# Kernel optimization log

Hardware: AMD Instinct MI355X
Metric: run time of the kernel (lower is better)

## Reference

```python
import jax, jax.numpy as jnp
from jax import lax
import numpy as np

EPS = 1e-5

def chan_ln(x, g, b):
    # LayerNorm over channel dim of NCHW
    mu = jnp.mean(x, axis=1, keepdims=True)
    var = jnp.mean((x - mu) ** 2, axis=1, keepdims=True)
    return (x - mu) / jnp.sqrt(var + EPS) * g[None, :, None, None] + b[None, :, None, None]

def selective_scan(dts, Bs, Cs, us, A):
    # dts, us: (B,K,C,L); Bs, Cs: (B,K,N,L); A: (K,C,N)
    def step(h, inp):
        dt_t, B_t, C_t, u_t = inp
        dA = jnp.exp(dt_t[..., None] * A)                     # (B,K,C,N)
        h = h * dA + (dt_t * u_t)[..., None] * B_t[:, :, None, :]
        y = jnp.einsum('bkcn,bkn->bkc', h, C_t)
        return h, y
    h0 = jnp.zeros(dts.shape[:-1] + (A.shape[-1],), dts.dtype)
    seq = (jnp.moveaxis(dts, -1, 0), jnp.moveaxis(Bs, -1, 0),
           jnp.moveaxis(Cs, -1, 0), jnp.moveaxis(us, -1, 0))
    _, ys = lax.scan(step, h0, seq)
    return jnp.moveaxis(ys, 0, -1)                            # (B,K,C,L)

def ss2d_core(x, x_proj_w, dt_proj_w, dt_proj_b, A_log, Ds):
    Bb, C, H, W = x.shape
    L = H * W
    R = dt_proj_w.shape[-1]
    N = A_log.shape[-1]
    x_flat = x.reshape(Bb, C, L)
    x_tr = jnp.transpose(x, (0, 1, 3, 2)).reshape(Bb, C, L)
    x_hwwh = jnp.stack([x_flat, x_tr], axis=1)                # (B,2,C,L)
    xs = jnp.concatenate([x_hwwh, jnp.flip(x_hwwh, axis=-1)], axis=1)  # (B,4,C,L)
    x_dbl = jnp.einsum('bkcl,kdc->bkdl', xs, x_proj_w)        # d = R+2N
    dts, Bs, Cs = jnp.split(x_dbl, [R, R + N], axis=2)
    dts = jnp.einsum('bkrl,kcr->bkcl', dts, dt_proj_w) + dt_proj_b[None, :, :, None]
    dts = jax.nn.softplus(dts)
    A = -jnp.exp(A_log)
    ys = selective_scan(dts, Bs, Cs, xs, A)
    ys = ys + xs * Ds[None, :, :, None]
    y0 = ys[:, 0]
    y1 = jnp.transpose(ys[:, 1].reshape(Bb, C, W, H), (0, 1, 3, 2)).reshape(Bb, C, L)
    yi = jnp.flip(ys[:, 2:], axis=-1)
    y2 = yi[:, 0]
    y3 = jnp.transpose(yi[:, 1].reshape(Bb, C, W, H), (0, 1, 3, 2)).reshape(Bb, C, L)
    return (y0 + y1 + y2 + y3).reshape(Bb, C, H, W)

def setup_inputs() -> dict:
    key = jax.random.key(0)
    ks = jax.random.split(key, 12)
    Hd, Di, N, R = 96, 192, 16, 6
    B, HH, WW = 2, 64, 64
    s = 0.02
    inp = {}
    inp['x'] = jax.random.normal(ks[0], (B, Hd, HH, WW), jnp.float32)
    inp['in_conv_w'] = s * jax.random.normal(ks[1], (Hd, Hd), jnp.float32)
    inp['ln1_g'] = jnp.ones((Hd,), jnp.float32)
    inp['ln1_b'] = jnp.zeros((Hd,), jnp.float32)
    inp['in_proj_w'] = s * jax.random.normal(ks[2], (Di, Hd), jnp.float32)
    inp['dw_w'] = s * jax.random.normal(ks[3], (Di, 1, 3, 3), jnp.float32)
    inp['dw_b'] = jnp.zeros((Di,), jnp.float32)
    inp['x_proj_w'] = s * jax.random.normal(ks[4], (4, R + 2 * N, Di), jnp.float32)
    inp['dt_proj_w'] = s * jax.random.normal(ks[5], (4, Di, R), jnp.float32)
    inp['dt_proj_b'] = 0.01 * jax.random.normal(ks[6], (4, Di), jnp.float32)
    inp['A_log'] = jnp.log(jnp.broadcast_to(jnp.arange(1.0, N + 1.0, dtype=jnp.float32), (4, Di, N)))
    inp['Ds'] = jnp.ones((4, Di), jnp.float32)
    inp['out_norm_g'] = jnp.ones((Di,), jnp.float32)
    inp['out_norm_b'] = jnp.zeros((Di,), jnp.float32)
    inp['out_proj_w'] = s * jax.random.normal(ks[7], (Hd, Di), jnp.float32)
    inp['skip_scale'] = jnp.ones((1,), jnp.float32)
    return inp

def reference(x, in_conv_w, ln1_g, ln1_b, in_proj_w, dw_w, dw_b, x_proj_w,
              dt_proj_w, dt_proj_b, A_log, Ds, out_norm_g, out_norm_b,
              out_proj_w, skip_scale):
    x1 = jnp.einsum('oi,bihw->bohw', in_conv_w, x)            # in_conv 1x1
    x1 = chan_ln(x1, ln1_g, ln1_b)
    skip = x1
    h = jnp.einsum('oi,bihw->bohw', in_proj_w, x1)            # in_proj 1x1
    h = lax.conv_general_dilated(h, dw_w, (1, 1), 'SAME',
                                 dimension_numbers=('NCHW', 'OIHW', 'NCHW'),
                                 feature_group_count=h.shape[1])
    h = h + dw_b[None, :, None, None]
    h = jax.nn.silu(h)
    y = ss2d_core(h, x_proj_w, dt_proj_w, dt_proj_b, A_log, Ds)
    y = chan_ln(y, out_norm_g, out_norm_b)
    out = jnp.einsum('oi,bihw->bohw', out_proj_w, y)
    return out + skip * skip_scale[0]
```

## Files before the change

kernel.cpp:

```cpp
#include <hip/hip_runtime.h>
#include <hip/hip_bf16.h>

#define Bb 2
#define HD 96
#define DI 192
#define LL 4096
#define Kd 4
#define Ns 16
#define Rr 6
#define SEG 256
#define SEGLEN 16
#define NBKCN (Bb*Kd*DI*Ns)
#define LNEPS 1e-5f
#define RW 40
#define LOG2E 1.44269504f

__global__ __launch_bounds__(384) void k_fused_in(const float* __restrict__ x,
    const float* __restrict__ w1, const float* __restrict__ g, const float* __restrict__ be,
    const float* __restrict__ w2, float* __restrict__ x1, float* __restrict__ hp) {
  __shared__ float xs[16][100];
  __shared__ float t1[16][100];
  __shared__ float red[2][16][24];
  int t = threadIdx.x;
  int l0 = blockIdx.x*16; int b = blockIdx.y;
  for (int idx=t; idx<HD*16; idx+=384) {
    int c = idx>>4, i = idx&15;
    xs[i][c] = x[((size_t)b*HD + c)*LL + l0 + i];
  }
  __syncthreads();
  int l = t & 15, cg = t >> 4;
  float a0=0.f,a1=0.f,a2=0.f,a3=0.f;
  {
    const float4* xr = (const float4*)&xs[l][0];
    const float4* wr0 = (const float4*)(w1 + (size_t)(cg*4+0)*HD);
    const float4* wr1 = (const float4*)(w1 + (size_t)(cg*4+1)*HD);
    const float4* wr2 = (const float4*)(w1 + (size_t)(cg*4+2)*HD);
    const float4* wr3 = (const float4*)(w1 + (size_t)(cg*4+3)*HD);
    #pragma unroll 6
    for (int j=0;j<24;j++) {
      float4 xv = xr[j];
      float4 v0 = wr0[j], v1 = wr1[j], v2 = wr2[j], v3 = wr3[j];
      a0 += xv.x*v0.x + xv.y*v0.y + xv.z*v0.z + xv.w*v0.w;
      a1 += xv.x*v1.x + xv.y*v1.y + xv.z*v1.z + xv.w*v1.w;
      a2 += xv.x*v2.x + xv.y*v2.y + xv.z*v2.z + xv.w*v2.w;
      a3 += xv.x*v3.x + xv.y*v3.y + xv.z*v3.z + xv.w*v3.w;
    }
  }
  float s = a0+a1+a2+a3;
  float s2 = a0*a0+a1*a1+a2*a2+a3*a3;
  red[0][l][cg]=s; red[1][l][cg]=s2;
  __syncthreads();
  float S=0.f, S2=0.f;
  #pragma unroll
  for (int q=0;q<24;q++) { S += red[0][l][q]; S2 += red[1][l][q]; }
  float mu = S*(1.f/HD);
  float var = S2*(1.f/HD) - mu*mu;
  float r = rsqrtf(var + LNEPS);
  {
    int c0 = cg*4;
    float v0 = (a0-mu)*r*g[c0+0] + be[c0+0];
    float v1 = (a1-mu)*r*g[c0+1] + be[c0+1];
    float v2 = (a2-mu)*r*g[c0+2] + be[c0+2];
    float v3 = (a3-mu)*r*g[c0+3] + be[c0+3];
    t1[l][c0+0]=v0; t1[l][c0+1]=v1; t1[l][c0+2]=v2; t1[l][c0+3]=v3;
    size_t ob = ((size_t)b*HD + c0)*LL + l0 + l;
    x1[ob]=v0; x1[ob+LL]=v1; x1[ob+2*(size_t)LL]=v2; x1[ob+3*(size_t)LL]=v3;
  }
  __syncthreads();
  float acc[8];
  #pragma unroll
  for (int q=0;q<8;q++) acc[q]=0.f;
  {
    const float4* yr = (const float4*)&t1[l][0];
    #pragma unroll 4
    for (int j=0;j<24;j++) {
      float4 yv = yr[j];
      #pragma unroll
      for (int q=0;q<8;q++) {
        float4 wv = ((const float4*)(w2 + (size_t)(cg*8+q)*HD))[j];
        acc[q] += yv.x*wv.x + yv.y*wv.y + yv.z*wv.z + yv.w*wv.w;
      }
    }
  }
  #pragma unroll
  for (int q=0;q<8;q++)
    hp[((size_t)b*DI + cg*8+q)*LL + l0 + l] = acc[q];
}

__global__ __launch_bounds__(192) void k_dwconv_silu_t(const float* __restrict__ hp,
    const float* __restrict__ wgt, const float* __restrict__ bias, float* __restrict__ v_t) {
  __shared__ float lds[24*65];
  int t = threadIdx.x;
  int w0 = t & 63, dg = t >> 6;
  int h = blockIdx.x, dq = blockIdx.y, b = blockIdx.z;
  for (int dd=0; dd<8; ++dd) {
    int dl = dg*8 + dd;
    int d = dq*24 + dl;
    const float* src = hp + ((size_t)b*DI + d)*LL;
    const float* wk = wgt + d*9;
    float acc = bias[d];
    #pragma unroll
    for (int dy=-1; dy<=1; dy++) {
      int hh = h+dy;
      if (hh < 0 || hh >= 64) continue;
      #pragma unroll
      for (int dx=-1; dx<=1; dx++) {
        int ww = w0+dx;
        if (ww < 0 || ww >= 64) continue;
        acc += wk[(dy+1)*3 + (dx+1)] * src[hh*64 + ww];
      }
    }
    lds[dl*65 + w0] = acc / (1.f + __expf(-acc));
  }
  __syncthreads();
  int hc = t % 24, ig = t / 24;
  if (ig < 8) {
    for (int ii=0; ii<8; ii++) {
      int i = ig*8 + ii;
      v_t[((size_t)b*LL + h*64 + i)*DI + dq*24 + hc] = lds[hc*65 + i];
    }
  }
}

__global__ __launch_bounds__(512) void k_proj(const float* __restrict__ v_t,
    const float* __restrict__ xpw, float* __restrict__ dblp) {
  __shared__ float lds[64*196];
  int t = threadIdx.x;
  int pt = blockIdx.x, k = blockIdx.y, b = blockIdx.z;
  const float4* src = (const float4*)(v_t + ((size_t)b*LL + pt*64)*DI);
  for (int idx=t; idx<64*48; idx+=512) {
    int p = idx/48, q = idx - p*48;
    *((float4*)&lds[p*196 + 4*q]) = src[idx];
  }
  __syncthreads();
  int p = t & 63, dg = t >> 6;
  int d0 = (dg<6) ? dg*5 : 30 + (dg-6)*4;
  int nd = (dg<6) ? 5 : 4;
  float acc[5];
  #pragma unroll
  for (int q=0;q<5;q++) acc[q]=0.f;
  const float4* W4 = (const float4*)(xpw + (size_t)(k*38 + d0)*DI);
  const float4* row4 = (const float4*)(lds + p*196);
  for (int c4=0;c4<48;c4++) {
    float4 xv = row4[c4];
    #pragma unroll
    for (int dd=0;dd<5;dd++) {
      if (dd < nd) {
        float4 wv = W4[(size_t)dd*48 + c4];
        acc[dd] += xv.x*wv.x + xv.y*wv.y + xv.z*wv.z + xv.w*wv.w;
      }
    }
  }
  float* o = dblp + (((size_t)b*4 + k)*LL + pt*64 + p)*RW;
  for (int dd=0;dd<nd;dd++) {
    int d = d0 + dd;
    o[d + ((d>=6)?2:0)] = acc[dd];
  }
}

__device__ __forceinline__ void dir_map(int k, int s, int& pbase, int& pstr) {
  if (k==0)      { pbase = s*16;                          pstr = 1;   }
  else if (k==1) { pbase = (s&3)*1024 + (s>>2);           pstr = 64;  }
  else if (k==2) { pbase = 4095 - s*16;                   pstr = -1;  }
  else           { pbase = 4095 - (s&3)*1024 - (s>>2);    pstr = -64; }
}

__device__ __forceinline__ float softplus_f(float raw) {
  float e = __expf(raw);
  float l = __logf(1.f + e);
  return (raw > 20.f) ? raw : l;
}

__global__ __launch_bounds__(384) void k_scanA(const float* __restrict__ v_t,
    const float* __restrict__ dblp, const float* __restrict__ dtw,
    const float* __restrict__ dtb, const float* __restrict__ A_log,
    float* __restrict__ hend, float* __restrict__ sdt_o) {
  __shared__ float uld[2][SEGLEN][DI];
  __shared__ float rows[2][SEGLEN][24];
  int t = threadIdx.x;
  int sub = t/192, tl = t - sub*192;
  int s = blockIdx.x*2 + sub;
  int k = blockIdx.y, b = blockIdx.z;
  int bk = b*4 + k;
  int pbase, pstr; dir_map(k, s, pbase, pstr);
  #pragma unroll
  for (int i=0;i<4;i++) {
    int idx = tl + i*192;
    int row = idx/48, q = idx - row*48;
    int p = pbase + row*pstr;
    const float4* src = (const float4*)(v_t + ((size_t)b*LL + p)*DI) + q;
    *((float4*)&uld[sub][row][4*q]) = *src;
  }
  if (tl < 96) {
    int r = tl/6, q = tl - r*6;
    const float4* src = (const float4*)(dblp + ((size_t)bk*LL + pbase + r*pstr)*RW);
    *((float4*)&rows[sub][r][4*q]) = src[q];
  }
  int c = tl;
  float w[6];
  {
    const float* wr = dtw + ((size_t)k*DI + c)*Rr;
    #pragma unroll
    for (int r=0;r<6;r++) w[r] = wr[r];
  }
  float bias = dtb[k*DI + c];
  float A2[16];
  {
    const float4* Ap = (const float4*)(A_log + ((size_t)k*DI + c)*Ns);
    #pragma unroll
    for (int q=0;q<4;q++) {
      float4 av = Ap[q];
      A2[4*q+0]=-__expf(av.x)*LOG2E; A2[4*q+1]=-__expf(av.y)*LOG2E;
      A2[4*q+2]=-__expf(av.z)*LOG2E; A2[4*q+3]=-__expf(av.w)*LOG2E;
    }
  }
  __syncthreads();
  float dtv[SEGLEN], duv[SEGLEN];
  float sdt = 0.f;
  #pragma unroll
  for (int j=0;j<SEGLEN;j++) {
    const float* row = &rows[sub][j][0];
    float4 d0 = *((const float4*)row);
    float2 d1 = *((const float2*)(row+4));
    float raw = bias + w[0]*d0.x + w[1]*d0.y + w[2]*d0.z + w[3]*d0.w
              + w[4]*d1.x + w[5]*d1.y;
    float dt = softplus_f(raw);
    dtv[j] = dt;
    duv[j] = dt * uld[sub][j][c];
    sdt += dt;
  }
  float h[16];
  #pragma unroll
  for (int n=0;n<16;n++) h[n]=0.f;
  #pragma unroll
  for (int j=0;j<SEGLEN;j++) {
    float dt = dtv[j], du = duv[j];
    const float4* Bv = (const float4*)(&rows[sub][j][8]);
    #pragma unroll
    for (int q=0;q<4;q++) {
      float4 bv = Bv[q];
      h[4*q+0] = h[4*q+0]*__builtin_amdgcn_exp2f(dt*A2[4*q+0]) + du*bv.x;
      h[4*q+1] = h[4*q+1]*__builtin_amdgcn_exp2f(dt*A2[4*q+1]) + du*bv.y;
      h[4*q+2] = h[4*q+2]*__builtin_amdgcn_exp2f(dt*A2[4*q+2]) + du*bv.z;
      h[4*q+3] = h[4*q+3]*__builtin_amdgcn_exp2f(dt*A2[4*q+3]) + du*bv.w;
    }
  }
  float* ho = hend + ((size_t)s*8 + bk)*(DI*Ns) + c;
  #pragma unroll
  for (int n=0;n<16;n++) ho[(size_t)n*DI] = h[n];
  sdt_o[((size_t)s*8 + bk)*DI + c] = sdt;
}

__global__ __launch_bounds__(64) void k_fix(float* __restrict__ hend,
    const float* __restrict__ sdt, const float* __restrict__ A_log) {
  int t = blockIdx.x*64 + threadIdx.x;
  int c = t % DI;
  int nn = (t / DI) & 15;
  int bk = t / (DI*Ns);
  int k = bk & 3;
  float A = -__expf(A_log[((size_t)k*DI + c)*Ns + nn]);
  float hi = 0.f;
  #pragma unroll 8
  for (int s=0; s<SEG; s++) {
    float he = hend[(size_t)s*NBKCN + t];
    float P  = __expf(A * sdt[(size_t)s*(8*DI) + bk*DI + c]);
    hend[(size_t)s*NBKCN + t] = hi;
    hi = he + P*hi;
  }
}

__global__ __launch_bounds__(384) void k_scanB(const float* __restrict__ v_t,
    const float* __restrict__ dblp, const float* __restrict__ dtw,
    const float* __restrict__ dtb, const float* __restrict__ A_log,
    const float* __restrict__ hinit, float* __restrict__ ym) {
  __shared__ float uld[2][SEGLEN][DI];
  __shared__ float rows[2][SEGLEN][RW];
  int t = threadIdx.x;
  int sub = t/192, tl = t - sub*192;
  int s = blockIdx.x*2 + sub;
  int k = blockIdx.y, b = blockIdx.z;
  int bk = b*4 + k;
  int pbase, pstr; dir_map(k, s, pbase, pstr);
  #pragma unroll
  for (int i=0;i<4;i++) {
    int idx = tl + i*192;
    int row = idx/48, q = idx - row*48;
    int p = pbase + row*pstr;
    const float4* src = (const float4*)(v_t + ((size_t)b*LL + p)*DI) + q;
    *((float4*)&uld[sub][row][4*q]) = *src;
  }
  if (tl < 160) {
    int r = tl/10, q = tl - r*10;
    const float4* src = (const float4*)(dblp + ((size_t)bk*LL + pbase + r*pstr)*RW);
    *((float4*)&rows[sub][r][4*q]) = src[q];
  }
  int c = tl;
  float w[6];
  {
    const float* wr = dtw + ((size_t)k*DI + c)*Rr;
    #pragma unroll
    for (int r=0;r<6;r++) w[r] = wr[r];
  }
  float bias = dtb[k*DI + c];
  float A2[16];
  {
    const float4* Ap = (const float4*)(A_log + ((size_t)k*DI + c)*Ns);
    #pragma unroll
    for (int q=0;q<4;q++) {
      float4 av = Ap[q];
      A2[4*q+0]=-__expf(av.x)*LOG2E; A2[4*q+1]=-__expf(av.y)*LOG2E;
      A2[4*q+2]=-__expf(av.z)*LOG2E; A2[4*q+3]=-__expf(av.w)*LOG2E;
    }
  }
  float h[16];
  {
    const float* hi = hinit + ((size_t)s*8 + bk)*(DI*Ns) + c;
    #pragma unroll
    for (int n=0;n<16;n++) h[n] = hi[(size_t)n*DI];
  }
  __syncthreads();
  float dtv[SEGLEN], duv[SEGLEN];
  #pragma unroll
  for (int j=0;j<SEGLEN;j++) {
    const float* row = &rows[sub][j][0];
    float4 d0 = *((const float4*)row);
    float2 d1 = *((const float2*)(row+4));
    float raw = bias + w[0]*d0.x + w[1]*d0.y + w[2]*d0.z + w[3]*d0.w
              + w[4]*d1.x + w[5]*d1.y;
    float dt = softplus_f(raw);
    dtv[j] = dt;
    duv[j] = dt * uld[sub][j][c];
  }
  float* ymk = ym + ((size_t)(k*Bb + b)*LL)*DI;
  #pragma unroll
  for (int j=0;j<SEGLEN;j++) {
    float dt = dtv[j], du = duv[j];
    const float4* Bv = (const float4*)(&rows[sub][j][8]);
    const float4* Cv = (const float4*)(&rows[sub][j][24]);
    float y = 0.f;
    #pragma unroll
    for (int q=0;q<4;q++) {
      float4 bv = Bv[q];
      float4 cv = Cv[q];
      h[4*q+0] = h[4*q+0]*__builtin_amdgcn_exp2f(dt*A2[4*q+0]) + du*bv.x;
      h[4*q+1] = h[4*q+1]*__builtin_amdgcn_exp2f(dt*A2[4*q+1]) + du*bv.y;
      h[4*q+2] = h[4*q+2]*__builtin_amdgcn_exp2f(dt*A2[4*q+2]) + du*bv.z;
      h[4*q+3] = h[4*q+3]*__builtin_amdgcn_exp2f(dt*A2[4*q+3]) + du*bv.w;
      y += h[4*q+0]*cv.x + h[4*q+1]*cv.y + h[4*q+2]*cv.z + h[4*q+3]*cv.w;
    }
    int p = pbase + j*pstr;
    ymk[(size_t)p*DI + c] = y;
  }
}

__global__ __launch_bounds__(384) void k_merge_out(const float* __restrict__ ym,
    const float* __restrict__ v_t, const float* __restrict__ Ds,
    const float* __restrict__ g, const float* __restrict__ be,
    const float* __restrict__ w3, const float* __restrict__ x1,
    const float* __restrict__ ss, float* __restrict__ out) {
  __shared__ float tile2[16*196];
  __shared__ float red[2][16][6];
  int t = threadIdx.x;
  int b = blockIdx.y;
  int l0 = blockIdx.x*16;
  int pp = t / 192, c = t - pp*192;
  int wv = t >> 6;
  int ln = t & 63;
  float sd = Ds[c] + Ds[DI+c] + Ds[2*DI+c] + Ds[3*DI+c];
  float gg = g[c], bb = be[c];
  float v[8];
  #pragma unroll
  for (int j=0;j<8;j++) {
    int i = 2*j + pp;
    size_t row = ((size_t)b*LL + l0 + i)*DI + c;
    float vv = ym[row] + ym[(size_t)2*LL*DI + row]
             + ym[(size_t)4*LL*DI + row] + ym[(size_t)6*LL*DI + row]
             + v_t[row]*sd;
    v[j] = vv;
    float s = vv, s2 = vv*vv;
    #pragma unroll
    for (int d=1; d<64; d<<=1) { s += __shfl_xor(s,d); s2 += __shfl_xor(s2,d); }
    if (ln==0) { red[0][i][wv]=s; red[1][i][wv]=s2; }
  }
  __syncthreads();
  #pragma unroll
  for (int j=0;j<8;j++) {
    int i = 2*j + pp;
    int w0i = pp*3;
    float S  = red[0][i][w0i]+red[0][i][w0i+1]+red[0][i][w0i+2];
    float S2 = red[1][i][w0i]+red[1][i][w0i+1]+red[1][i][w0i+2];
    float mu = S*(1.f/DI);
    float var = S2*(1.f/DI) - mu*mu;
    float r = rsqrtf(var + LNEPS);
    tile2[i*196 + c] = (v[j]-mu)*r*gg + bb;
  }
  __syncthreads();
  int l = t & 15, og = t >> 4;
  float a0=0.f,a1=0.f,a2=0.f,a3=0.f;
  {
    const float4* yr = (const float4*)&tile2[l*196];
    const float4* wr0 = (const float4*)(w3 + (size_t)(og*4+0)*DI);
    const float4* wr1 = (const float4*)(w3 + (size_t)(og*4+1)*DI);
    const float4* wr2 = (const float4*)(w3 + (size_t)(og*4+2)*DI);
    const float4* wr3 = (const float4*)(w3 + (size_t)(og*4+3)*DI);
    #pragma unroll 6
    for (int j=0;j<48;j++) {
      float4 yv = yr[j];
      float4 v0 = wr0[j], v1 = wr1[j], v2 = wr2[j], v3 = wr3[j];
      a0 += yv.x*v0.x + yv.y*v0.y + yv.z*v0.z + yv.w*v0.w;
      a1 += yv.x*v1.x + yv.y*v1.y + yv.z*v1.z + yv.w*v1.w;
      a2 += yv.x*v2.x + yv.y*v2.y + yv.z*v2.z + yv.w*v2.w;
      a3 += yv.x*v3.x + yv.y*v3.y + yv.z*v3.z + yv.w*v3.w;
    }
  }
  float sc = ss[0];
  int o0 = og*4;
  size_t ob = ((size_t)b*HD + o0)*LL + l0 + l;
  out[ob]            = a0 + x1[ob]*sc;
  out[ob+LL]         = a1 + x1[ob+LL]*sc;
  out[ob+2*(size_t)LL] = a2 + x1[ob+2*(size_t)LL]*sc;
  out[ob+3*(size_t)LL] = a3 + x1[ob+3*(size_t)LL]*sc;
}

extern "C" void kernel_launch(void* const* d_in, const int* in_sizes, int n_in,
                              void* d_out, int out_size, void* d_ws, size_t ws_size,
                              hipStream_t stream) {
  const float* x         = (const float*)d_in[0];
  const float* in_conv_w = (const float*)d_in[1];
  const float* ln1_g     = (const float*)d_in[2];
  const float* ln1_b     = (const float*)d_in[3];
  const float* in_proj_w = (const float*)d_in[4];
  const float* dw_w      = (const float*)d_in[5];
  const float* dw_b      = (const float*)d_in[6];
  const float* x_proj_w  = (const float*)d_in[7];
  const float* dt_proj_w = (const float*)d_in[8];
  const float* dt_proj_b = (const float*)d_in[9];
  const float* A_log     = (const float*)d_in[10];
  const float* Ds        = (const float*)d_in[11];
  const float* onorm_g   = (const float*)d_in[12];
  const float* onorm_b   = (const float*)d_in[13];
  const float* out_proj_w= (const float*)d_in[14];
  const float* skip_s    = (const float*)d_in[15];
  float* out = (float*)d_out;

  float* ws   = (float*)d_ws;
  float* x1   = ws;
  float* hp   = x1   + 786432;
  float* v_t  = hp   + 1572864;
  float* dblp = v_t  + 1572864;
  float* hend = dblp + 1310720;
  float* sdt  = hend + 6291456;
  float* ym   = sdt  + 393216;

  k_fused_in<<<dim3(LL/16, Bb), dim3(384), 0, stream>>>(x, in_conv_w, ln1_g, ln1_b, in_proj_w, x1, hp);
  k_dwconv_silu_t<<<dim3(64, 8, Bb), dim3(192), 0, stream>>>(hp, dw_w, dw_b, v_t);
  k_proj   <<<dim3(LL/64, Kd, Bb), dim3(512), 0, stream>>>(v_t, x_proj_w, dblp);
  k_scanA  <<<dim3(SEG/2, Kd, Bb), dim3(384), 0, stream>>>(v_t, dblp, dt_proj_w, dt_proj_b, A_log, hend, sdt);
  k_fix    <<<dim3(NBKCN/64), dim3(64), 0, stream>>>(hend, sdt, A_log);
  k_scanB  <<<dim3(SEG/2, Kd, Bb), dim3(384), 0, stream>>>(v_t, dblp, dt_proj_w, dt_proj_b, A_log, hend, ym);
  k_merge_out<<<dim3(LL/16, Bb), dim3(384), 0, stream>>>(ym, v_t, Ds, onorm_g, onorm_b, out_proj_w, x1, skip_s, out);
}
```

Measured before the change: 278.0 us.

## Merge scan phases into one cooperative persistent kernel with grid syncs

The three scan kernels (segment-local scan, cross-segment carry fix, and the final scan with output) are fused into one cooperative kernel. It launches 512 blocks of 192 threads that loop over tasks and are separated by grid.sync(). This removes two kernel launch boundaries. In exchange it adds grid-wide barrier cost and a fixed grid size that may underuse the GPU, especially in the fix phase, which has only NBKCN/192 threads' worth of work spread across the grid.

```diff
diff --git a/kernel.cpp b/kernel.cpp
--- a/kernel.cpp
+++ b/kernel.cpp
@@ -1,5 +1,8 @@
 #include <hip/hip_runtime.h>
+#include <hip/hip_cooperative_groups.h>
 #include <hip/hip_bf16.h>
+
+namespace cg = cooperative_groups;
 
 #define Bb 2
 #define HD 96
@@ -10,6 +13,7 @@
 #define Rr 6
 #define SEG 256
 #define SEGLEN 16
+#define NTASK (SEG*Kd*Bb)
 #define NBKCN (Bb*Kd*DI*Ns)
 #define LNEPS 1e-5f
 #define RW 40
@@ -28,14 +32,14 @@
     xs[i][c] = x[((size_t)b*HD + c)*LL + l0 + i];
   }
   __syncthreads();
-  int l = t & 15, cg = t >> 4;
+  int l = t & 15, cg0 = t >> 4;
   float a0=0.f,a1=0.f,a2=0.f,a3=0.f;
   {
     const float4* xr = (const float4*)&xs[l][0];
-    const float4* wr0 = (const float4*)(w1 + (size_t)(cg*4+0)*HD);
-    const float4* wr1 = (const float4*)(w1 + (size_t)(cg*4+1)*HD);
-    const float4* wr2 = (const float4*)(w1 + (size_t)(cg*4+2)*HD);
-    const float4* wr3 = (const float4*)(w1 + (size_t)(cg*4+3)*HD);
+    const float4* wr0 = (const float4*)(w1 + (size_t)(cg0*4+0)*HD);
+    const float4* wr1 = (const float4*)(w1 + (size_t)(cg0*4+1)*HD);
+    const float4* wr2 = (const float4*)(w1 + (size_t)(cg0*4+2)*HD);
+    const float4* wr3 = (const float4*)(w1 + (size_t)(cg0*4+3)*HD);
     #pragma unroll 6
     for (int j=0;j<24;j++) {
       float4 xv = xr[j];
@@ -48,7 +52,7 @@
   }
   float s = a0+a1+a2+a3;
   float s2 = a0*a0+a1*a1+a2*a2+a3*a3;
-  red[0][l][cg]=s; red[1][l][cg]=s2;
+  red[0][l][cg0]=s; red[1][l][cg0]=s2;
   __syncthreads();
   float S=0.f, S2=0.f;
   #pragma unroll
@@ -57,7 +61,7 @@
   float var = S2*(1.f/HD) - mu*mu;
   float r = rsqrtf(var + LNEPS);
   {
-    int c0 = cg*4;
+    int c0 = cg0*4;
     float v0 = (a0-mu)*r*g[c0+0] + be[c0+0];
     float v1 = (a1-mu)*r*g[c0+1] + be[c0+1];
     float v2 = (a2-mu)*r*g[c0+2] + be[c0+2];
@@ -77,14 +81,14 @@
       float4 yv = yr[j];
       #pragma unroll
       for (int q=0;q<8;q++) {
-        float4 wv = ((const float4*)(w2 + (size_t)(cg*8+q)*HD))[j];
+        float4 wv = ((const float4*)(w2 + (size_t)(cg0*8+q)*HD))[j];
         acc[q] += yv.x*wv.x + yv.y*wv.y + yv.z*wv.z + yv.w*wv.w;
       }
     }
   }
   #pragma unroll
   for (int q=0;q<8;q++)
-    hp[((size_t)b*DI + cg*8+q)*LL + l0 + l] = acc[q];
+    hp[((size_t)b*DI + cg0*8+q)*LL + l0 + l] = acc[q];
 }
 
 __global__ __launch_bounds__(192) void k_dwconv_silu_t(const float* __restrict__ hp,
@@ -171,185 +175,179 @@
   return (raw > 20.f) ? raw : l;
 }
 
-__global__ __launch_bounds__(384) void k_scanA(const float* __restrict__ v_t,
-    const float* __restrict__ dblp, const float* __restrict__ dtw,
-    const float* __restrict__ dtb, const float* __restrict__ A_log,
-    float* __restrict__ hend, float* __restrict__ sdt_o) {
-  __shared__ float uld[2][SEGLEN][DI];
-  __shared__ float rows[2][SEGLEN][24];
+__global__ __launch_bounds__(192, 3) void k_scan_all(
+    const float* __restrict__ v_t, const float* __restrict__ dblp,
+    const float* __restrict__ dtw, const float* __restrict__ dtb,
+    const float* __restrict__ A_log, float* __restrict__ hend,
+    float* __restrict__ sdt_o, float* __restrict__ ym) {
+  cg::grid_group grid = cg::this_grid();
+  __shared__ float uld[SEGLEN][DI];
+  __shared__ float rows[SEGLEN][RW];
   int t = threadIdx.x;
-  int sub = t/192, tl = t - sub*192;
-  int s = blockIdx.x*2 + sub;
-  int k = blockIdx.y, b = blockIdx.z;
-  int bk = b*4 + k;
-  int pbase, pstr; dir_map(k, s, pbase, pstr);
-  #pragma unroll
-  for (int i=0;i<4;i++) {
-    int idx = tl + i*192;
-    int row = idx/48, q = idx - row*48;
-    int p = pbase + row*pstr;
-    const float4* src = (const float4*)(v_t + ((size_t)b*LL + p)*DI) + q;
-    *((float4*)&uld[sub][row][4*q]) = *src;
-  }
-  if (tl < 96) {
-    int r = tl/6, q = tl - r*6;
-    const float4* src = (const float4*)(dblp + ((size_t)bk*LL + pbase + r*pstr)*RW);
-    *((float4*)&rows[sub][r][4*q]) = src[q];
-  }
-  int c = tl;
-  float w[6];
-  {
-    const float* wr = dtw + ((size_t)k*DI + c)*Rr;
-    #pragma unroll
-    for (int r=0;r<6;r++) w[r] = wr[r];
-  }
-  float bias = dtb[k*DI + c];
-  float A2[16];
-  {
-    const float4* Ap = (const float4*)(A_log + ((size_t)k*DI + c)*Ns);
-    #pragma unroll
-    for (int q=0;q<4;q++) {
-      float4 av = Ap[q];
-      A2[4*q+0]=-__expf(av.x)*LOG2E; A2[4*q+1]=-__expf(av.y)*LOG2E;
-      A2[4*q+2]=-__expf(av.z)*LOG2E; A2[4*q+3]=-__expf(av.w)*LOG2E;
-    }
-  }
-  __syncthreads();
-  float dtv[SEGLEN], duv[SEGLEN];
-  float sdt = 0.f;
-  #pragma unroll
-  for (int j=0;j<SEGLEN;j++) {
-    const float* row = &rows[sub][j][0];
-    float4 d0 = *((const float4*)row);
-    float2 d1 = *((const float2*)(row+4));
-    float raw = bias + w[0]*d0.x + w[1]*d0.y + w[2]*d0.z + w[3]*d0.w
-              + w[4]*d1.x + w[5]*d1.y;
-    float dt = softplus_f(raw);
-    dtv[j] = dt;
-    duv[j] = dt * uld[sub][j][c];
-    sdt += dt;
-  }
-  float h[16];
-  #pragma unroll
-  for (int n=0;n<16;n++) h[n]=0.f;
-  #pragma unroll
-  for (int j=0;j<SEGLEN;j++) {
-    float dt = dtv[j], du = duv[j];
-    const float4* Bv = (const float4*)(&rows[sub][j][8]);
-    #pragma unroll
-    for (int q=0;q<4;q++) {
-      float4 bv = Bv[q];
-      h[4*q+0] = h[4*q+0]*__builtin_amdgcn_exp2f(dt*A2[4*q+0]) + du*bv.x;
-      h[4*q+1] = h[4*q+1]*__builtin_amdgcn_exp2f(dt*A2[4*q+1]) + du*bv.y;
-      h[4*q+2] = h[4*q+2]*__builtin_amdgcn_exp2f(dt*A2[4*q+2]) + du*bv.z;
-      h[4*q+3] = h[4*q+3]*__builtin_amdgcn_exp2f(dt*A2[4*q+3]) + du*bv.w;
-    }
-  }
-  float* ho = hend + ((size_t)s*8 + bk)*(DI*Ns) + c;
-  #pragma unroll
-  for (int n=0;n<16;n++) ho[(size_t)n*DI] = h[n];
-  sdt_o[((size_t)s*8 + bk)*DI + c] = sdt;
-}
-
-__global__ __launch_bounds__(64) void k_fix(float* __restrict__ hend,
-    const float* __restrict__ sdt, const float* __restrict__ A_log) {
-  int t = blockIdx.x*64 + threadIdx.x;
-  int c = t % DI;
-  int nn = (t / DI) & 15;
-  int bk = t / (DI*Ns);
-  int k = bk & 3;
-  float A = -__expf(A_log[((size_t)k*DI + c)*Ns + nn]);
-  float hi = 0.f;
-  #pragma unroll 8
-  for (int s=0; s<SEG; s++) {
-    float he = hend[(size_t)s*NBKCN + t];
-    float P  = __expf(A * sdt[(size_t)s*(8*DI) + bk*DI + c]);
-    hend[(size_t)s*NBKCN + t] = hi;
-    hi = he + P*hi;
-  }
-}
-
-__global__ __launch_bounds__(384) void k_scanB(const float* __restrict__ v_t,
-    const float* __restrict__ dblp, const float* __restrict__ dtw,
-    const float* __restrict__ dtb, const float* __restrict__ A_log,
-    const float* __restrict__ hinit, float* __restrict__ ym) {
-  __shared__ float uld[2][SEGLEN][DI];
-  __shared__ float rows[2][SEGLEN][RW];
-  int t = threadIdx.x;
-  int sub = t/192, tl = t - sub*192;
-  int s = blockIdx.x*2 + sub;
-  int k = blockIdx.y, b = blockIdx.z;
-  int bk = b*4 + k;
-  int pbase, pstr; dir_map(k, s, pbase, pstr);
-  #pragma unroll
-  for (int i=0;i<4;i++) {
-    int idx = tl + i*192;
-    int row = idx/48, q = idx - row*48;
-    int p = pbase + row*pstr;
-    const float4* src = (const float4*)(v_t + ((size_t)b*LL + p)*DI) + q;
-    *((float4*)&uld[sub][row][4*q]) = *src;
-  }
-  if (tl < 160) {
-    int r = tl/10, q = tl - r*10;
-    const float4* src = (const float4*)(dblp + ((size_t)bk*LL + pbase + r*pstr)*RW);
-    *((float4*)&rows[sub][r][4*q]) = src[q];
-  }
-  int c = tl;
-  float w[6];
-  {
-    const float* wr = dtw + ((size_t)k*DI + c)*Rr;
-    #pragma unroll
-    for (int r=0;r<6;r++) w[r] = wr[r];
-  }
-  float bias = dtb[k*DI + c];
-  float A2[16];
-  {
-    const float4* Ap = (const float4*)(A_log + ((size_t)k*DI + c)*Ns);
-    #pragma unroll
-    for (int q=0;q<4;q++) {
-      float4 av = Ap[q];
-      A2[4*q+0]=-__expf(av.x)*LOG2E; A2[4*q+1]=-__expf(av.y)*LOG2E;
-      A2[4*q+2]=-__expf(av.z)*LOG2E; A2[4*q+3]=-__expf(av.w)*LOG2E;
-    }
-  }
-  float h[16];
-  {
-    const float* hi = hinit + ((size_t)s*8 + bk)*(DI*Ns) + c;
-    #pragma unroll
-    for (int n=0;n<16;n++) h[n] = hi[(size_t)n*DI];
-  }
-  __syncthreads();
-  float dtv[SEGLEN], duv[SEGLEN];
-  #pragma unroll
-  for (int j=0;j<SEGLEN;j++) {
-    const float* row = &rows[sub][j][0];
-    float4 d0 = *((const float4*)row);
-    float2 d1 = *((const float2*)(row+4));
-    float raw = bias + w[0]*d0.x + w[1]*d0.y + w[2]*d0.z + w[3]*d0.w
-              + w[4]*d1.x + w[5]*d1.y;
-    float dt = softplus_f(raw);
-    dtv[j] = dt;
-    duv[j] = dt * uld[sub][j][c];
-  }
-  float* ymk = ym + ((size_t)(k*Bb + b)*LL)*DI;
-  #pragma unroll
-  for (int j=0;j<SEGLEN;j++) {
-    float dt = dtv[j], du = duv[j];
-    const float4* Bv = (const float4*)(&rows[sub][j][8]);
-    const float4* Cv = (const float4*)(&rows[sub][j][24]);
-    float y = 0.f;
-    #pragma unroll
-    for (int q=0;q<4;q++) {
-      float4 bv = Bv[q];
-      float4 cv = Cv[q];
-      h[4*q+0] = h[4*q+0]*__builtin_amdgcn_exp2f(dt*A2[4*q+0]) + du*bv.x;
-      h[4*q+1] = h[4*q+1]*__builtin_amdgcn_exp2f(dt*A2[4*q+1]) + du*bv.y;
-      h[4*q+2] = h[4*q+2]*__builtin_amdgcn_exp2f(dt*A2[4*q+2]) + du*bv.z;
-      h[4*q+3] = h[4*q+3]*__builtin_amdgcn_exp2f(dt*A2[4*q+3]) + du*bv.w;
-      y += h[4*q+0]*cv.x + h[4*q+1]*cv.y + h[4*q+2]*cv.z + h[4*q+3]*cv.w;
-    }
-    int p = pbase + j*pstr;
-    ymk[(size_t)p*DI + c] = y;
+  int c = t;
+
+  for (int task = blockIdx.x; task < NTASK; task += gridDim.x) {
+    int s = task & (SEG-1);
+    int k = (task >> 8) & 3;
+    int b = task >> 10;
+    int bk = b*4 + k;
+    int pbase, pstr; dir_map(k, s, pbase, pstr);
+    __syncthreads();
+    #pragma unroll
+    for (int i=0;i<4;i++) {
+      int idx = t + i*192;
+      int row = idx/48, q = idx - row*48;
+      int p = pbase + row*pstr;
+      *((float4*)&uld[row][4*q]) = ((const float4*)(v_t + ((size_t)b*LL + p)*DI))[q];
+    }
+    if (t < 96) {
+      int r = t/6, q = t - r*6;
+      *((float4*)&rows[r][4*q]) = ((const float4*)(dblp + ((size_t)bk*LL + pbase + r*pstr)*RW))[q];
+    }
+    float w[6];
+    {
+      const float* wr = dtw + ((size_t)k*DI + c)*Rr;
+      #pragma unroll
+      for (int r=0;r<6;r++) w[r] = wr[r];
+    }
+    float bias = dtb[k*DI + c];
+    float A2[16];
+    {
+      const float4* Ap = (const float4*)(A_log + ((size_t)k*DI + c)*Ns);
+      #pragma unroll
+      for (int q=0;q<4;q++) {
+        float4 av = Ap[q];
+        A2[4*q+0]=-__expf(av.x)*LOG2E; A2[4*q+1]=-__expf(av.y)*LOG2E;
+        A2[4*q+2]=-__expf(av.z)*LOG2E; A2[4*q+3]=-__expf(av.w)*LOG2E;
+      }
+    }
+    __syncthreads();
+    float dtv[SEGLEN], duv[SEGLEN];
+    float sdt = 0.f;
+    #pragma unroll
+    for (int j=0;j<SEGLEN;j++) {
+      const float* row = &rows[j][0];
+      float4 d0 = *((const float4*)row);
+      float2 d1 = *((const float2*)(row+4));
+      float raw = bias + w[0]*d0.x + w[1]*d0.y + w[2]*d0.z + w[3]*d0.w
+                + w[4]*d1.x + w[5]*d1.y;
+      float dt = softplus_f(raw);
+      dtv[j] = dt;
+      duv[j] = dt * uld[j][c];
+      sdt += dt;
+    }
+    float h[16];
+    #pragma unroll
+    for (int n=0;n<16;n++) h[n]=0.f;
+    #pragma unroll
+    for (int j=0;j<SEGLEN;j++) {
+      float dt = dtv[j], du = duv[j];
+      const float4* Bv = (const float4*)(&rows[j][8]);
+      #pragma unroll
+      for (int q=0;q<4;q++) {
+        float4 bv = Bv[q];
+        h[4*q+0] = h[4*q+0]*__builtin_amdgcn_exp2f(dt*A2[4*q+0]) + du*bv.x;
+        h[4*q+1] = h[4*q+1]*__builtin_amdgcn_exp2f(dt*A2[4*q+1]) + du*bv.y;
+        h[4*q+2] = h[4*q+2]*__builtin_amdgcn_exp2f(dt*A2[4*q+2]) + du*bv.z;
+        h[4*q+3] = h[4*q+3]*__builtin_amdgcn_exp2f(dt*A2[4*q+3]) + du*bv.w;
+      }
+    }
+    float* ho = hend + ((size_t)s*8 + bk)*(DI*Ns) + c;
+    #pragma unroll
+    for (int n=0;n<16;n++) ho[(size_t)n*DI] = h[n];
+    sdt_o[((size_t)s*8 + bk)*DI + c] = sdt;
+  }
+  grid.sync();
+  for (int gix = blockIdx.x*192 + t; gix < NBKCN; gix += gridDim.x*192) {
+    int cc = gix % DI;
+    int nn = (gix / DI) & 15;
+    int bk = gix / (DI*Ns);
+    int k = bk & 3;
+    float A = -__expf(A_log[((size_t)k*DI + cc)*Ns + nn]);
+    float hi = 0.f;
+    #pragma unroll 8
+    for (int s=0; s<SEG; s++) {
+      float he = hend[(size_t)s*NBKCN + gix];
+      float P  = __expf(A * sdt_o[(size_t)s*(8*DI) + bk*DI + cc]);
+      hend[(size_t)s*NBKCN + gix] = hi;
+      hi = he + P*hi;
+    }
+  }
+  grid.sync();
+  for (int task = blockIdx.x; task < NTASK; task += gridDim.x) {
+    int s = task & (SEG-1);
+    int k = (task >> 8) & 3;
+    int b = task >> 10;
+    int bk = b*4 + k;
+    int pbase, pstr; dir_map(k, s, pbase, pstr);
+    __syncthreads();
+    #pragma unroll
+    for (int i=0;i<4;i++) {
+      int idx = t + i*192;
+      int row = idx/48, q = idx - row*48;
+      int p = pbase + row*pstr;
+      *((float4*)&uld[row][4*q]) = ((const float4*)(v_t + ((size_t)b*LL + p)*DI))[q];
+    }
+    if (t < 160) {
+      int r = t/10, q = t - r*10;
+      *((float4*)&rows[r][4*q]) = ((const float4*)(dblp + ((size_t)bk*LL + pbase + r*pstr)*RW))[q];
+    }
+    float w[6];
+    {
+      const float* wr = dtw + ((size_t)k*DI + c)*Rr;
+      #pragma unroll
+      for (int r=0;r<6;r++) w[r] = wr[r];
+    }
+    float bias = dtb[k*DI + c];
+    float A2[16];
+    {
+      const float4* Ap = (const float4*)(A_log + ((size_t)k*DI + c)*Ns);
+      #pragma unroll
+      for (int q=0;q<4;q++) {
+        float4 av = Ap[q];
+        A2[4*q+0]=-__expf(av.x)*LOG2E; A2[4*q+1]=-__expf(av.y)*LOG2E;
+        A2[4*q+2]=-__expf(av.z)*LOG2E; A2[4*q+3]=-__expf(av.w)*LOG2E;
+      }
+    }
+    float h[16];
+    {
+      const float* hi = hend + ((size_t)s*8 + bk)*(DI*Ns) + c;
+      #pragma unroll
+      for (int n=0;n<16;n++) h[n] = hi[(size_t)n*DI];
+    }
+    __syncthreads();
+    float dtv[SEGLEN], duv[SEGLEN];
+    #pragma unroll
+    for (int j=0;j<SEGLEN;j++) {
+      const float* row = &rows[j][0];
+      float4 d0 = *((const float4*)row);
+      float2 d1 = *((const float2*)(row+4));
+      float raw = bias + w[0]*d0.x + w[1]*d0.y + w[2]*d0.z + w[3]*d0.w
+                + w[4]*d1.x + w[5]*d1.y;
+      float dt = softplus_f(raw);
+      dtv[j] = dt;
+      duv[j] = dt * uld[j][c];
+    }
+    float* ymk = ym + ((size_t)(k*Bb + b)*LL)*DI;
+    #pragma unroll
+    for (int j=0;j<SEGLEN;j++) {
+      float dt = dtv[j], du = duv[j];
+      const float4* Bv = (const float4*)(&rows[j][8]);
+      const float4* Cv = (const float4*)(&rows[j][24]);
+      float y = 0.f;
+      #pragma unroll
+      for (int q=0;q<4;q++) {
+        float4 bv = Bv[q];
+        float4 cv = Cv[q];
+        h[4*q+0] = h[4*q+0]*__builtin_amdgcn_exp2f(dt*A2[4*q+0]) + du*bv.x;
+        h[4*q+1] = h[4*q+1]*__builtin_amdgcn_exp2f(dt*A2[4*q+1]) + du*bv.y;
+        h[4*q+2] = h[4*q+2]*__builtin_amdgcn_exp2f(dt*A2[4*q+2]) + du*bv.z;
+        h[4*q+3] = h[4*q+3]*__builtin_amdgcn_exp2f(dt*A2[4*q+3]) + du*bv.w;
+        y += h[4*q+0]*cv.x + h[4*q+1]*cv.y + h[4*q+2]*cv.z + h[4*q+3]*cv.w;
+      }
+      int p = pbase + j*pstr;
+      ymk[(size_t)p*DI + c] = y;
+    }
   }
 }
 
@@ -455,8 +453,17 @@
   k_fused_in<<<dim3(LL/16, Bb), dim3(384), 0, stream>>>(x, in_conv_w, ln1_g, ln1_b, in_proj_w, x1, hp);
   k_dwconv_silu_t<<<dim3(64, 8, Bb), dim3(192), 0, stream>>>(hp, dw_w, dw_b, v_t);
   k_proj   <<<dim3(LL/64, Kd, Bb), dim3(512), 0, stream>>>(v_t, x_proj_w, dblp);
-  k_scanA  <<<dim3(SEG/2, Kd, Bb), dim3(384), 0, stream>>>(v_t, dblp, dt_proj_w, dt_proj_b, A_log, hend, sdt);
-  k_fix    <<<dim3(NBKCN/64), dim3(64), 0, stream>>>(hend, sdt, A_log);
-  k_scanB  <<<dim3(SEG/2, Kd, Bb), dim3(384), 0, stream>>>(v_t, dblp, dt_proj_w, dt_proj_b, A_log, hend, ym);
+  {
+    void* args[8];
+    args[0] = (void*)&v_t;
+    args[1] = (void*)&dblp;
+    args[2] = (void*)&dt_proj_w;
+    args[3] = (void*)&dt_proj_b;
+    args[4] = (void*)&A_log;
+    args[5] = (void*)&hend;
+    args[6] = (void*)&sdt;
+    args[7] = (void*)&ym;
+    hipLaunchCooperativeKernel((void*)k_scan_all, dim3(512), dim3(192), args, 0, stream);
+  }
   k_merge_out<<<dim3(LL/16, Bb), dim3(384), 0, stream>>>(ym, v_t, Ds, onorm_g, onorm_b, out_proj_w, x1, skip_s, out);
 }
```

After: 438.5 us. 1.58x slower.
